# Kernel tuning notes

Measured on AMD Instinct MI355X. Metric: run time of the kernel, lower is better.

The kernel has to match this reference:

```python
import jax, jax.numpy as jnp
import numpy as np

B, T = 16, 100
MCL = 100      # MAX_CODE_LEN
D_IN = 200     # input_dim (= ques_encoding)
D_BERT = 768
KC = 50        # KC_one_hot_dim
KCD = 100      # kc_embed_dim
HID = 128
SCALE_BERT = 100
TW = 0.5       # QPALA_config.total_attention_weight
BTW = 0.5      # BLAA_config.total_attention_weight


def setup_inputs():
    key = jax.random.key(0)
    ks = jax.random.split(key, 20)
    f32 = jnp.float32
    # composite input feature vector: [ques_enc | code2vec idx | bert | time | score | kc one-hot]
    rnn_first = (jax.random.uniform(ks[0], (B, T, D_IN)) < 0.1).astype(f32)
    c2v = jax.random.randint(ks[1], (B, T, 3 * MCL), 0, 10000).astype(f32)
    bert = jax.random.normal(ks[2], (B, T, D_BERT), f32)
    time_f = jax.random.uniform(ks[3], (B, T, 10), f32)
    score_f = jax.random.uniform(ks[4], (B, T, 2), f32)
    kc = (jax.random.uniform(ks[5], (B, T, KC)) < 0.15).astype(f32)
    x = jnp.concatenate([rnn_first, c2v, bert, time_f, score_f, kc], axis=2)  # [B,T,1330]
    s = 0.05
    p = lambda k, shp: jax.random.normal(k, shp, f32) * s
    return dict(
        x=x,
        node_emb=p(ks[6], (10002, 100)),
        path_emb=p(ks[7], (20002, 100)),
        Wb=p(ks[8], (SCALE_BERT, D_BERT)), bb=jnp.zeros((SCALE_BERT,), f32),
        Wna=p(ks[9], (500, 500)), bna=jnp.zeros((500,), f32),
        Wia=p(ks[10], (KCD, 500)), bia=jnp.zeros((KCD,), f32),
        Wattn=p(ks[11], (1, 500)), battn=jnp.zeros((1,), f32),
        kc_emb=p(ks[12], (KC, KCD)),
        Wt=p(ks[13], (1, SCALE_BERT + KC + KCD)), bt=jnp.zeros((1,), f32),
        Wih=p(ks[14], (4 * HID, 950)), Whh=p(ks[15], (4 * HID, HID)),
        bih=jnp.zeros((4 * HID,), f32), bhh=jnp.zeros((4 * HID,), f32),
        Wfc=p(ks[16], (100, HID + KC + D_IN)), bfc=jnp.zeros((100,), f32),
    )


def _lstm(xseq, Wih, Whh, bih, bhh):
    # PyTorch LSTM, gate order i,f,g,o; batch_first
    bsz = xseq.shape[0]
    pre = jnp.einsum('btd,gd->btg', xseq, Wih) + bih + bhh  # [B,T,4H]

    def step(carry, g_in):
        h, c = carry
        g = g_in + h @ Whh.T
        i, f, gg, o = jnp.split(g, 4, axis=-1)
        c = jax.nn.sigmoid(f) * c + jax.nn.sigmoid(i) * jnp.tanh(gg)
        h = jax.nn.sigmoid(o) * jnp.tanh(c)
        return (h, c), h

    init = (jnp.zeros((bsz, HID), xseq.dtype), jnp.zeros((bsz, HID), xseq.dtype))
    _, hs = jax.lax.scan(step, init, jnp.swapaxes(pre, 0, 1))
    return jnp.swapaxes(hs, 0, 1)


def _forward(x, node_emb, path_emb, Wb, bb, Wna, bna, Wia, bia, Wattn, battn,
             kc_emb, Wt, bt, Wih, Whh, bih, bhh, Wfc, bfc):
    b, t = x.shape[0], x.shape[1]
    rnn_first = x[:, :, :D_IN]
    bert = x[:, :, 500:500 + D_BERT]
    kc_part = x[:, :, 1280:1280 + KC]
    c2v = x[:, :, D_IN:D_IN + 3 * MCL].reshape(b, t, MCL, 3).astype(jnp.int32)
    # gather embeddings + broadcast encoding -> full_embed [B,T,MCL,500]
    full = jnp.concatenate([
        node_emb[c2v[..., 0]], node_emb[c2v[..., 2]], path_emb[c2v[..., 1]],
        jnp.broadcast_to(rnn_first[:, :, None, :], (b, t, MCL, D_IN))], axis=3)
    bert_vec = bert @ Wb.T + bb  # [B,T,100]
    # non-interactive attention pooling (NB: original softmaxes over dim=1 = time)
    cw = jnp.tanh(full @ Wna.T + bna) @ Wattn.T + battn  # [B,T,MCL,1]
    aw = jax.nn.softmax(cw, axis=1)
    na = jnp.sum(full * aw, axis=2)  # [B,T,500]
    kcn = jnp.sum(kc_part, axis=2, keepdims=True)
    kcn = jnp.where(kcn == 0, 1.0, kcn)
    # interactive (KC) cross attention
    trans = full @ Wia.T + bia  # [B,T,MCL,KCD]
    Q = kc_part[..., None] * kc_emb[None, None]  # [B,T,KC,KCD]
    attn = jax.nn.softmax(jnp.einsum('btkd,btmd->btkm', Q, trans), axis=-1)
    Hm = jnp.einsum('btkm,btmd->btkd', attn, trans) * kc_part[..., None]
    ia = jnp.sum(Hm, axis=2) / kcn  # [B,T,KCD]
    rnn_input = jnp.concatenate([kc_part, rnn_first, ia, na, bert_vec], axis=2)  # [B,T,950]
    lstm_out = _lstm(rnn_input, Wih, Whh, bih, bhh)  # [B,T,HID]
    # per-time-step causal attention over lstm_out (vectorized form of the python loop)
    w = (jnp.concatenate([bert_vec, kc_part, ia], axis=2) @ Wt.T + bt)[..., 0]  # [B,T]
    mask = jnp.tril(jnp.ones((t, t), bool))
    logits = jnp.where(mask[None], w[:, None, :], -1e30)
    cattn = jax.nn.softmax(logits, axis=-1)  # [B,T,T]
    cur = jnp.einsum('bij,bjh->bih', cattn, lstm_out)
    attended = lstm_out * (1.0 - TW)
    attended = attended.at[:, 0].set(lstm_out[:, 0])
    idx = jnp.arange(t)
    addm = ((idx >= 1) & (idx <= t - 2)).astype(x.dtype)[None, :, None]
    attended = attended + cur * BTW * addm
    out = jax.nn.sigmoid(
        jnp.concatenate([rnn_first, kc_part, attended], axis=2) @ Wfc.T + bfc)
    return out  # [B,T,100]


def reference(x, node_emb, path_emb, Wb, bb, Wna, bna, Wia, bia, Wattn, battn,
              kc_emb, Wt, bt, Wih, Whh, bih, bhh, Wfc, bfc):
    return _forward(x, node_emb, path_emb, Wb, bb, Wna, bna, Wia, bia, Wattn, battn,
                    kc_emb, Wt, bt, Wih, Whh, bih, bhh, Wfc, bfc)
```

## Files before the change

### kernel.cpp

```cpp
#include <hip/hip_runtime.h>
#include <math.h>

typedef unsigned short ushort_t;
typedef __attribute__((ext_vector_type(8))) short bf16x8;
typedef __attribute__((ext_vector_type(4))) float f32x4;

constexpr int CB = 16, CT = 100, CMCL = 100, CDIN = 200;
constexpr int CKC = 50, CHID = 128;
constexpr int XCH = 1330;
constexpr int NBT = CB * CT;
constexpr int NNODE = 10002, NPATH = 20002;
constexpr int TRS = 114;
constexpr int HSTR = 136;
constexpr int NODE_W = 1408;
constexpr int PATH_W = 768;
constexpr int XR_W   = 640;

__device__ __forceinline__ float frcp(float v){ return __builtin_amdgcn_rcpf(v); }
__device__ __forceinline__ float fsigmoid(float v){ return frcp(1.f + __expf(-v)); }
__device__ __forceinline__ float ftanh_(float v){
  float e = __expf(-2.f*fabsf(v));
  return copysignf((1.f - e) * frcp(1.f + e), v);
}
__device__ __forceinline__ float wredsum(float v){
  #pragma unroll
  for (int off = 32; off; off >>= 1) v += __shfl_xor(v, off);
  return v;
}
__device__ __forceinline__ float wredmax(float v){
  #pragma unroll
  for (int off = 32; off; off >>= 1) v = fmaxf(v, __shfl_xor(v, off));
  return v;
}
__device__ __forceinline__ ushort_t f2b(float f){
  union { float f; unsigned u; } c{f};
  return (ushort_t)((c.u + 0x7FFFu + ((c.u >> 16) & 1u)) >> 16);
}
__device__ __forceinline__ float b2f(unsigned hbits){
  union { unsigned u; float f; } c{hbits << 16};
  return c.f;
}
__device__ __forceinline__ void b8f(const ushort_t* p, float* o){
  uint4 v = *reinterpret_cast<const uint4*>(p);
  o[0]=b2f(v.x & 0xFFFFu); o[1]=b2f(v.x >> 16);
  o[2]=b2f(v.y & 0xFFFFu); o[3]=b2f(v.y >> 16);
  o[4]=b2f(v.z & 0xFFFFu); o[5]=b2f(v.z >> 16);
  o[6]=b2f(v.w & 0xFFFFu); o[7]=b2f(v.w >> 16);
}

struct GDesc {
  const float* A; const float* B; float* Cf; ushort_t* Cb;
  int lda, kOff, kMax, K, M, Npad, rbp, cb, nsplit, ldc, blocks;
};
struct MegaArgs { GDesc d[4]; int nd; };

__global__ __launch_bounds__(256) void mega_gemm(MegaArgs args)
{
  constexpr int KS = 136;
  __shared__ ushort_t As[128*KS];
  __shared__ ushort_t Bs[128*KS];
  int id = blockIdx.x;
  int di = 0;
  while (di < args.nd-1 && id >= args.d[di].blocks) { id -= args.d[di].blocks; ++di; }
  GDesc g = args.d[di];
  const int per = g.rbp * g.cb;
  const int sp = id / per, r = id % per;
  const int xcd = r & 7, s2 = r >> 3;
  const int y = xcd + 8*(s2 / g.cb), cbi = s2 % g.cb;
  const int bm = y*128, bn = cbi*128;
  if (bm >= g.M) return;
  const int tid = threadIdx.x, lane = tid & 63, w = tid >> 6;
  const int wm = w & 1, wn = w >> 1;
  const int lr = lane & 15, lkq = lane >> 4;
  const int kbase = g.kOff + sp * g.K;
  const int hK = g.K >> 1;

  for (int f = tid; f < 128*hK; f += 256) {
    int row = f / hK, j2 = (f % hK)*2;
    int gm = bm + row;
    float2 va = make_float2(0.f,0.f);
    if (gm < g.M && kbase + j2 + 2 <= g.kMax)
      va = *reinterpret_cast<const float2*>(g.A + (long)gm*g.lda + kbase + j2);
    *reinterpret_cast<unsigned*>(&As[row*KS + j2]) = (unsigned)f2b(va.x) | ((unsigned)f2b(va.y)<<16);
    float2 vb = *reinterpret_cast<const float2*>(g.B + ((long)sp*g.Npad + bn + row)*g.K + j2);
    *reinterpret_cast<unsigned*>(&Bs[row*KS + j2]) = (unsigned)f2b(vb.x) | ((unsigned)f2b(vb.y)<<16);
  }
  const int padw = (128 - g.K) >> 1;
  for (int f = tid; f < 128*padw; f += 256) {
    int row = f / padw, jd = f % padw;
    *reinterpret_cast<unsigned*>(&As[row*KS + g.K + jd*2]) = 0u;
    *reinterpret_cast<unsigned*>(&Bs[row*KS + g.K + jd*2]) = 0u;
  }
  __syncthreads();

  f32x4 acc[4][4];
  #pragma unroll
  for (int i = 0; i < 4; ++i)
    #pragma unroll
    for (int j = 0; j < 4; ++j) acc[i][j] = f32x4{0.f,0.f,0.f,0.f};
  #pragma unroll
  for (int ks = 0; ks < 4; ++ks) {
    const int ko = ks*32 + lkq*8;
    bf16x8 af[4], bf[4];
    #pragma unroll
    for (int i = 0; i < 4; ++i)
      af[i] = *reinterpret_cast<const bf16x8*>(&As[(wm*64 + i*16 + lr)*KS + ko]);
    #pragma unroll
    for (int j = 0; j < 4; ++j)
      bf[j] = *reinterpret_cast<const bf16x8*>(&Bs[(wn*64 + j*16 + lr)*KS + ko]);
    #pragma unroll
    for (int i = 0; i < 4; ++i)
      #pragma unroll
      for (int j = 0; j < 4; ++j)
        acc[i][j] = __builtin_amdgcn_mfma_f32_16x16x32_bf16(af[i], bf[j], acc[i][j], 0, 0, 0);
  }
  #pragma unroll
  for (int i = 0; i < 4; ++i) {
    #pragma unroll
    for (int j = 0; j < 4; ++j) {
      #pragma unroll
      for (int rr = 0; rr < 4; ++rr) {
        int gr = bm + wm*64 + i*16 + lkq*4 + rr;
        int gc = bn + wn*64 + j*16 + lr;
        if (gr < g.M) {
          if (g.Cb) g.Cb[(long)gr * g.ldc + gc] = f2b(acc[i][j][rr]);
          else      g.Cf[((long)sp*g.M + gr)*g.ldc + gc] = acc[i][j][rr];
        }
      }
    }
  }
}

__global__ void pack_Bn(const float* __restrict__ Wna, const float* __restrict__ Wia, float* __restrict__ Bn)
{
  int i = blockIdx.x*256 + threadIdx.x;
  if (i >= NODE_W*100) return;
  int n = i / 100, k = i % 100;
  float v = 0.f;
  if (n < 500)                      v = Wna[(long)n*500 + k];
  else if (n >= 512 && n < 1012)    v = Wna[(long)(n-512)*500 + 100 + k];
  else if (n >= 1024 && n < 1124)   v = (k == n-1024) ? 1.f : 0.f;
  else if (n >= 1136 && n < 1236)   v = Wia[(long)(n-1136)*500 + k];
  else if (n >= 1248 && n < 1348)   v = Wia[(long)(n-1248)*500 + 100 + k];
  Bn[i] = v;
}
__global__ void pack_Bp(const float* __restrict__ Wna, const float* __restrict__ Wia, float* __restrict__ Bp)
{
  int i = blockIdx.x*256 + threadIdx.x;
  if (i >= PATH_W*100) return;
  int n = i / 100, k = i % 100;
  float v = 0.f;
  if (n < 500)                    v = Wna[(long)n*500 + 200 + k];
  else if (n >= 512 && n < 612)   v = (k == n-512) ? 1.f : 0.f;
  else if (n >= 624 && n < 724)   v = Wia[(long)(n-624)*500 + 200 + k];
  Bp[i] = v;
}
__global__ void pack_XB2(const float* __restrict__ Wna, const float* __restrict__ Wia,
                         const float* __restrict__ bna, const float* __restrict__ bia,
                         float* __restrict__ XB2, float* __restrict__ bias_x)
{
  int i = blockIdx.x*256 + threadIdx.x;
  if (i < XR_W) {
    float b = 0.f;
    if (i < 500) b = bna[i];
    else if (i >= 512 && i < 612) b = bia[i-512];
    bias_x[i] = b;
  }
  if (i >= 2*XR_W*100) return;
  int s = i / (XR_W*100), n = (i / 100) % XR_W, k = i % 100;
  int k2 = s*100 + k;
  float v = 0.f;
  if (n < 500)                  v = Wna[(long)n*500 + 300 + k2];
  else if (n >= 512 && n < 612) v = Wia[(long)(n-512)*500 + 300 + k2];
  XB2[i] = v;
}
__global__ void pack_bertB(const float* __restrict__ Wb, float* __restrict__ BertB)
{
  int i = blockIdx.x*256 + threadIdx.x;
  if (i >= 6*128*128) return;
  int s = i / (128*128), n = (i / 128) % 128, k = i % 128;
  BertB[i] = (n < 100) ? Wb[(long)n*768 + s*128 + k] : 0.f;
}
__global__ void pack_P2B(const float* __restrict__ Wih, float* __restrict__ P2B)
{
  int i = blockIdx.x*256 + threadIdx.x;
  if (i >= 10*512*96) return;
  int s = i / (512*96), n = (i / 96) % 512, k = i % 96;
  int kg = s*96 + k;
  P2B[i] = (kg < 950) ? Wih[(long)n*950 + kg] : 0.f;
}
__global__ void pack_wattn(const float* __restrict__ Wattn, ushort_t* __restrict__ wab)
{
  int i = blockIdx.x * 256 + threadIdx.x;
  if (i < 512) wab[i] = (i < 500) ? f2b(Wattn[i]) : (ushort_t)0;
}

__global__ __launch_bounds__(256) void reduce1(
    const float* __restrict__ xrP, const float* __restrict__ bias_x, ushort_t* __restrict__ XR,
    const float* __restrict__ bertP, const float* __restrict__ bb, float* __restrict__ rnn)
{
  int bt = blockIdx.x, tid = threadIdx.x;
  for (int c = tid; c < XR_W; c += 256) {
    float v = xrP[(long)bt*XR_W + c] + xrP[((long)NBT + bt)*XR_W + c] + bias_x[c];
    XR[(long)bt*XR_W + c] = f2b(v);
  }
  if (tid < 100) {
    float v = bb[tid];
    #pragma unroll
    for (int s = 0; s < 6; ++s) v += bertP[((long)s*NBT + bt)*128 + tid];
    rnn[(long)bt*950 + 850 + tid] = v;
  }
}

__global__ __launch_bounds__(512) void reduce_p2(
    const float* __restrict__ p2P, const float* __restrict__ bih, const float* __restrict__ bhh,
    ushort_t* __restrict__ P2)
{
  int bt = blockIdx.x, g = threadIdx.x;
  float v = bih[g] + bhh[g];
  #pragma unroll
  for (int s = 0; s < 10; ++s) v += p2P[((long)s*NBT + bt)*512 + g];
  int bq = bt / CT, tt = bt % CT;
  int q = g >> 7, rem = g & 127, ww = rem >> 4, lr2 = rem & 15;
  int lk2 = bq >> 2, rr = bq & 3;
  P2[((((long)tt*4 + q)*8 + ww)*4 + lk2)*64 + lr2*4 + rr] = f2b(v);
}

__global__ __launch_bounds__(256) void cw2_kernel(
    const float* __restrict__ x, const ushort_t* __restrict__ NODE_ALL,
    const ushort_t* __restrict__ PATH_ALL, const ushort_t* __restrict__ XR,
    const ushort_t* __restrict__ WAB,
    const float* __restrict__ battn, float* __restrict__ cwT)
{
  int bt = blockIdx.x, b = bt / CT, t = bt % CT;
  int tid = threadIdx.x, w = tid >> 6, lane = tid & 63;
  __shared__ int idx_s[300];
  for (int i = tid; i < 300; i += 256) idx_s[i] = (int)x[(long)bt*XCH + 200 + i];
  float rseg[8], wseg[8];
  b8f(XR + (long)bt*XR_W + lane*8, rseg);
  b8f(WAB + lane*8, wseg);
  __syncthreads();
  float bat = battn[0];

  uint4 A0, C0, P0, A1, C1, P1;
  auto issue = [&](int m, uint4& A, uint4& C, uint4& P){
    if (m < CMCL) {
      int ai = idx_s[3*m], pi = idx_s[3*m+1], ci = idx_s[3*m+2];
      A = *reinterpret_cast<const uint4*>(NODE_ALL + (long)ai*NODE_W + lane*8);
      C = *reinterpret_cast<const uint4*>(NODE_ALL + (long)ci*NODE_W + 512 + lane*8);
      P = *reinterpret_cast<const uint4*>(PATH_ALL + (long)pi*PATH_W + lane*8);
    }
  };
  auto proc = [&](int m, const uint4& A, const uint4& C, const uint4& P){
    if (m >= CMCL) return;
    const unsigned ua[4] = {A.x, A.y, A.z, A.w};
    const unsigned uc[4] = {C.x, C.y, C.z, C.w};
    const unsigned up[4] = {P.x, P.y, P.z, P.w};
    float acc = 0.f;
    #pragma unroll
    for (int jj = 0; jj < 4; ++jj) {
      float lo = b2f(ua[jj] & 0xffffu) + b2f(uc[jj] & 0xffffu) + b2f(up[jj] & 0xffffu) + rseg[2*jj];
      float hi = b2f(ua[jj] >> 16)     + b2f(uc[jj] >> 16)     + b2f(up[jj] >> 16)     + rseg[2*jj+1];
      acc = fmaf(ftanh_(lo), wseg[2*jj], acc);
      acc = fmaf(ftanh_(hi), wseg[2*jj+1], acc);
    }
    acc = wredsum(acc);
    if (lane == 0) cwT[((long)b*CMCL + m)*CT + t] = acc + bat;
  };

  issue(w, A0, C0, P0);
  for (int it = 0; it < 25; it += 2) {
    int m0 = w + it*4;
    issue(m0 + 4, A1, C1, P1);
    proc(m0, A0, C0, P0);
    issue(m0 + 8, A0, C0, P0);
    proc(m0 + 4, A1, C1, P1);
  }
}

__global__ void aw_kernel(const float* __restrict__ cwT, float* __restrict__ awT)
{
  int bm = blockIdx.x; int lane = threadIdx.x;
  const float* row = cwT + (long)bm * CT;
  bool h1 = lane < (CT - 64);
  float v0 = row[lane];
  float v1 = h1 ? row[64 + lane] : -3.0e38f;
  float mx = wredmax(fmaxf(v0, v1));
  float e0 = __expf(v0 - mx);
  float e1 = h1 ? __expf(v1 - mx) : 0.f;
  float s = wredsum(e0 + e1);
  float inv = frcp(s);
  awT[(long)bm*CT + lane] = e0 * inv;
  if (h1) awT[(long)bm*CT + 64 + lane] = e1 * inv;
}

__global__ __launch_bounds__(256) void fuse2_kernel(
    const float* __restrict__ x,
    const ushort_t* __restrict__ NODE_ALL, const ushort_t* __restrict__ PATH_ALL,
    const ushort_t* __restrict__ XR, const float* __restrict__ awT,
    const float* __restrict__ kc_emb, float* __restrict__ rnn)
{
  int bt = blockIdx.x, b = bt / CT, t = bt % CT;
  int tid = threadIdx.x, w = tid >> 6, lane = tid & 63;
  int sub = lane >> 5, li = lane & 31;

  __shared__ ushort_t tr_s[100*TRS];
  __shared__ float nacc[4][344];
  __shared__ float ia_red[4][104];
  __shared__ float aw_s[100];
  __shared__ int   idx_s[300];
  __shared__ float kcl[CKC];
  __shared__ int   act_k[CKC];
  __shared__ int   nact_s;
  __shared__ float kcn_s, awsum_s;

  for (int i = tid; i < 300; i += 256) idx_s[i] = (int)x[(long)bt*XCH + 200 + i];
  if (tid < 100) aw_s[tid] = awT[((long)b*CMCL + tid)*CT + t];
  if (tid < CKC) kcl[tid] = x[(long)bt*XCH + 1280 + tid];
  __syncthreads();
  if (tid == 0) {
    float kcn = 0.f; int na = 0;
    for (int k = 0; k < CKC; ++k) { float v = kcl[k]; kcn += v; if (v != 0.f) act_k[na++] = k; }
    nact_s = na; kcn_s = (kcn == 0.f) ? 1.f : kcn;
    float s = 0.f;
    for (int m = 0; m < CMCL; ++m) s += aw_s[m];
    awsum_s = s;
  }
  float rwseg[8];
  if (li >= 14 && li < 28) b8f(XR + (long)bt*XR_W + 512 + (li-14)*8, rwseg);
  __syncthreads();

  float na_a[8] = {}, na_c[8] = {}, na_p[8] = {};
  const bool gv = (li < 28);
  uint4 A0, C0, P0, A1, C1, P1;
  auto g_issue = [&](int m, uint4& A, uint4& C, uint4& P){
    if (m < CMCL && gv) {
      int ai = idx_s[3*m], pi = idx_s[3*m+1], ci = idx_s[3*m+2];
      int eo = li*8, uo = (li-14)*8;
      A = *reinterpret_cast<const uint4*>(NODE_ALL + (long)ai*NODE_W + 1024 + eo);
      C = *reinterpret_cast<const uint4*>(NODE_ALL + (long)ci*NODE_W + ((li<14) ? 1024 + eo : 1248 + uo));
      P = *reinterpret_cast<const uint4*>(PATH_ALL + (long)pi*PATH_W + 512 + eo);
    }
  };
  auto g_proc = [&](int m, const uint4& A, const uint4& C, const uint4& P){
    if (m >= CMCL || !gv) return;
    const unsigned ua[4] = {A.x, A.y, A.z, A.w};
    const unsigned uc[4] = {C.x, C.y, C.z, C.w};
    const unsigned up[4] = {P.x, P.y, P.z, P.w};
    if (li < 14) {
      float awm = aw_s[m];
      #pragma unroll
      for (int jj = 0; jj < 4; ++jj) {
        na_a[2*jj]   = fmaf(awm, b2f(ua[jj] & 0xffffu), na_a[2*jj]);
        na_a[2*jj+1] = fmaf(awm, b2f(ua[jj] >> 16),     na_a[2*jj+1]);
        na_c[2*jj]   = fmaf(awm, b2f(uc[jj] & 0xffffu), na_c[2*jj]);
        na_c[2*jj+1] = fmaf(awm, b2f(uc[jj] >> 16),     na_c[2*jj+1]);
        na_p[2*jj]   = fmaf(awm, b2f(up[jj] & 0xffffu), na_p[2*jj]);
        na_p[2*jj+1] = fmaf(awm, b2f(up[jj] >> 16),     na_p[2*jj+1]);
      }
    } else {
      unsigned* d32 = reinterpret_cast<unsigned*>(&tr_s[m*TRS + (li-14)*8]);
      #pragma unroll
      for (int jj = 0; jj < 4; ++jj) {
        float lo = b2f(ua[jj] & 0xffffu) + b2f(uc[jj] & 0xffffu) + b2f(up[jj] & 0xffffu) + rwseg[2*jj];
        float hi = b2f(ua[jj] >> 16)     + b2f(uc[jj] >> 16)     + b2f(up[jj] >> 16)     + rwseg[2*jj+1];
        d32[jj] = (unsigned)f2b(lo) | ((unsigned)f2b(hi) << 16);
      }
    }
  };
  const int mb = w*2 + sub;
  g_issue(mb, A0, C0, P0);
  for (int it = 0; it < 13; it += 2) {
    g_issue((it+1)*8 + mb, A1, C1, P1);
    g_proc(it*8 + mb, A0, C0, P0);
    g_issue((it+2)*8 + mb, A0, C0, P0);
    g_proc((it+1)*8 + mb, A1, C1, P1);
  }
  #pragma unroll
  for (int j = 0; j < 8; ++j) {
    na_a[j] += __shfl_xor(na_a[j], 32);
    na_c[j] += __shfl_xor(na_c[j], 32);
    na_p[j] += __shfl_xor(na_p[j], 32);
  }
  if (lane < 14) {
    #pragma unroll
    for (int j = 0; j < 8; ++j) {
      nacc[w][      lane*8 + j] = na_a[j];
      nacc[w][112 + lane*8 + j] = na_c[j];
      nacc[w][224 + lane*8 + j] = na_p[j];
    }
  }
  __syncthreads();

  for (int q = tid; q < 336; q += 256) {
    float v = nacc[0][q] + nacc[1][q] + nacc[2][q] + nacc[3][q];
    int seg = q / 112, col = q % 112;
    if (col < 100) rnn[(long)bt*950 + 350 + seg*100 + col] = v;
  }
  for (int q = tid; q < CDIN; q += 256) {
    float xv = x[(long)bt*XCH + q];
    rnn[(long)bt*950 + 50 + q] = xv;
    rnn[(long)bt*950 + 650 + q] = awsum_s * xv;
  }
  if (tid < CKC) rnn[(long)bt*950 + tid] = kcl[tid];

  float ia0 = 0.f, ia1 = 0.f;
  const bool vrow1 = lane < 36;
  const bool vpv   = lane < 50;
  const int nact = nact_s;
  const unsigned* tr32_0 = reinterpret_cast<const unsigned*>(&tr_s[lane*TRS]);
  const unsigned* tr32_1 = reinterpret_cast<const unsigned*>(&tr_s[(64+lane)*TRS]);
  const unsigned* tr32   = reinterpret_cast<const unsigned*>(tr_s);
  for (int ki = w; ki < nact; ki += 4) {
    int k = act_k[ki];
    float kck = kcl[k];
    const float* ke = kc_emb + (long)k*100;
    float s0 = 0.f, s1 = 0.f;
    #pragma unroll 5
    for (int dh = 0; dh < 50; ++dh) {
      float k0 = ke[2*dh], k1 = ke[2*dh+1];
      unsigned u0 = tr32_0[dh];
      s0 = fmaf(k0, b2f(u0 & 0xffffu), s0);
      s0 = fmaf(k1, b2f(u0 >> 16), s0);
      if (vrow1) {
        unsigned u1 = tr32_1[dh];
        s1 = fmaf(k0, b2f(u1 & 0xffffu), s1);
        s1 = fmaf(k1, b2f(u1 >> 16), s1);
      }
    }
    s0 *= kck; s1 *= kck;
    float mx = wredmax(fmaxf(s0, vrow1 ? s1 : -3.0e38f));
    float p0e = __expf(s0 - mx);
    float p1e = vrow1 ? __expf(s1 - mx) : 0.f;
    float sm = wredsum(p0e + p1e);
    float inv = kck * frcp(sm);
    p0e *= inv; p1e *= inv;
    #pragma unroll 4
    for (int m = 0; m < CMCL; ++m) {
      float pm = (m < 64) ? __shfl(p0e, m) : __shfl(p1e, m - 64);
      if (vpv) {
        unsigned u = tr32[m*57 + lane];
        ia0 = fmaf(pm, b2f(u & 0xffffu), ia0);
        ia1 = fmaf(pm, b2f(u >> 16), ia1);
      }
    }
  }
  if (vpv) { ia_red[w][2*lane] = ia0; ia_red[w][2*lane+1] = ia1; }
  __syncthreads();
  if (tid < 100) {
    float v = (ia_red[0][tid] + ia_red[1][tid] + ia_red[2][tid] + ia_red[3][tid]) * frcp(kcn_s);
    rnn[(long)bt*950 + 250 + tid] = v;
  }
}

__global__ __launch_bounds__(512) void lstm_mfma2(
    const ushort_t* __restrict__ P2,
    const float* __restrict__ Whh,
    float* __restrict__ lstm_out)
{
  const int tid = threadIdx.x, lane = tid & 63, w = tid >> 6;
  const int lr = lane & 15, lkq = lane >> 4;
  __shared__ ushort_t H[2][16 * HSTR];
  {
    ushort_t* hp = &H[0][0];
    for (int i = tid; i < 2*16*HSTR; i += 512) hp[i] = 0;
  }

  bf16x8 bw0[4], bw1[4], bw2[4], bw3[4];
  #pragma unroll
  for (int kk = 0; kk < 4; ++kk) {
    short s[8];
    const float* wp0 = Whh + (long)(0*128 + w*16 + lr) * 128 + kk*32 + lkq*8;
    const float* wp1 = Whh + (long)(1*128 + w*16 + lr) * 128 + kk*32 + lkq*8;
    const float* wp2 = Whh + (long)(2*128 + w*16 + lr) * 128 + kk*32 + lkq*8;
    const float* wp3 = Whh + (long)(3*128 + w*16 + lr) * 128 + kk*32 + lkq*8;
    #pragma unroll
    for (int j = 0; j < 8; ++j) s[j] = (short)f2b(wp0[j]);
    bw0[kk] = bf16x8{s[0],s[1],s[2],s[3],s[4],s[5],s[6],s[7]};
    #pragma unroll
    for (int j = 0; j < 8; ++j) s[j] = (short)f2b(wp1[j]);
    bw1[kk] = bf16x8{s[0],s[1],s[2],s[3],s[4],s[5],s[6],s[7]};
    #pragma unroll
    for (int j = 0; j < 8; ++j) s[j] = (short)f2b(wp2[j]);
    bw2[kk] = bf16x8{s[0],s[1],s[2],s[3],s[4],s[5],s[6],s[7]};
    #pragma unroll
    for (int j = 0; j < 8; ++j) s[j] = (short)f2b(wp3[j]);
    bw3[kk] = bf16x8{s[0],s[1],s[2],s[3],s[4],s[5],s[6],s[7]};
  }

  auto pptr = [&](int t, int q){
    return reinterpret_cast<const uint2*>(P2 + (((((long)t*4 + q)*8 + w)*4 + lkq)*64 + lr*4));
  };
  uint2 pc0 = *pptr(0,0), pc1 = *pptr(0,1), pc2 = *pptr(0,2), pc3 = *pptr(0,3);
  uint2 pn0, pn1, pn2, pn3;
  f32x4 c = {0.f,0.f,0.f,0.f};
  __syncthreads();

  int pb = 0;
  for (int t = 0; t < CT; ++t) {
    if (t + 1 < CT) { pn0 = *pptr(t+1,0); pn1 = *pptr(t+1,1); pn2 = *pptr(t+1,2); pn3 = *pptr(t+1,3); }
    bf16x8 a[4];
    #pragma unroll
    for (int kk = 0; kk < 4; ++kk)
      a[kk] = *reinterpret_cast<const bf16x8*>(&H[pb][lr*HSTR + kk*32 + lkq*8]);
    f32x4 acc0 = f32x4{ b2f(pc0.x & 0xffffu), b2f(pc0.x >> 16), b2f(pc0.y & 0xffffu), b2f(pc0.y >> 16) };
    f32x4 acc1 = f32x4{ b2f(pc1.x & 0xffffu), b2f(pc1.x >> 16), b2f(pc1.y & 0xffffu), b2f(pc1.y >> 16) };
    f32x4 acc2 = f32x4{ b2f(pc2.x & 0xffffu), b2f(pc2.x >> 16), b2f(pc2.y & 0xffffu), b2f(pc2.y >> 16) };
    f32x4 acc3 = f32x4{ b2f(pc3.x & 0xffffu), b2f(pc3.x >> 16), b2f(pc3.y & 0xffffu), b2f(pc3.y >> 16) };
    #pragma unroll
    for (int kk = 0; kk < 4; ++kk) {
      acc0 = __builtin_amdgcn_mfma_f32_16x16x32_bf16(a[kk], bw0[kk], acc0, 0,0,0);
      acc1 = __builtin_amdgcn_mfma_f32_16x16x32_bf16(a[kk], bw1[kk], acc1, 0,0,0);
      acc2 = __builtin_amdgcn_mfma_f32_16x16x32_bf16(a[kk], bw2[kk], acc2, 0,0,0);
      acc3 = __builtin_amdgcn_mfma_f32_16x16x32_bf16(a[kk], bw3[kk], acc3, 0,0,0);
    }
    #pragma unroll
    for (int r = 0; r < 4; ++r) {
      float ig = fsigmoid(acc0[r]);
      float fg = fsigmoid(acc1[r]);
      float gg = ftanh_(acc2[r]);
      float og = fsigmoid(acc3[r]);
      c[r] = fg*c[r] + ig*gg;
      float h = og * ftanh_(c[r]);
      int row = lkq*4 + r;
      H[pb^1][row*HSTR + w*16 + lr] = f2b(h);
      lstm_out[((long)row*CT + t)*128 + w*16 + lr] = h;
    }
    __syncthreads();
    pb ^= 1;
    pc0 = pn0; pc1 = pn1; pc2 = pn2; pc3 = pn3;
  }
}

__global__ void w_kernel(const float* __restrict__ rnn, const float* __restrict__ Wt,
                         const float* __restrict__ bt0, float* __restrict__ wbuf)
{
  int bt = blockIdx.x; int lane = threadIdx.x;
  float acc = 0.f;
  for (int i = lane; i < 250; i += 64) {
    float f;
    if (i < 100)      f = rnn[(long)bt*950 + 850 + i];
    else if (i < 150) f = rnn[(long)bt*950 + (i - 100)];
    else              f = rnn[(long)bt*950 + 250 + (i - 150)];
    acc = fmaf(Wt[i], f, acc);
  }
  acc = wredsum(acc);
  if (lane == 0) wbuf[bt] = acc + bt0[0];
}

__global__ void transpose_wfc(const float* __restrict__ Wfc, float* __restrict__ WfcT)
{
  int i = blockIdx.x*256 + threadIdx.x;
  if (i < 100*378) { int o = i / 378, q = i % 378; WfcT[q*100 + o] = Wfc[i]; }
}

__global__ __launch_bounds__(256) void final_kernel(
    const float* __restrict__ x, const float* __restrict__ wbuf,
    const float* __restrict__ lstm_out, const float* __restrict__ WfcT,
    const float* __restrict__ bfc, float* __restrict__ out)
{
  int bt = blockIdx.x; int b = bt / CT, i = bt % CT;
  int tid = threadIdx.x;
  __shared__ float p_s[CT];
  __shared__ float feat_s[384];
  if (tid < 64) {
    bool h1 = (64 + tid) < CT;
    float v0 = (tid <= i) ? wbuf[(long)b*CT + tid] : -3.0e38f;
    float v1 = (h1 && (64 + tid) <= i) ? wbuf[(long)b*CT + 64 + tid] : -3.0e38f;
    float mx = wredmax(fmaxf(v0, v1));
    float e0 = (tid <= i) ? __expf(v0 - mx) : 0.f;
    float e1 = (h1 && (64 + tid) <= i) ? __expf(v1 - mx) : 0.f;
    float s = wredsum(e0 + e1);
    float inv = frcp(s);
    p_s[tid] = e0 * inv;
    if (h1) p_s[64 + tid] = e1 * inv;
  }
  __syncthreads();
  if (tid < CHID) {
    float cur = 0.f;
    #pragma unroll 4
    for (int j = 0; j <= i; ++j) cur = fmaf(p_s[j], lstm_out[((long)b*CT + j)*CHID + tid], cur);
    float l = lstm_out[((long)b*CT + i)*CHID + tid];
    float att;
    if (i == 0) att = l;
    else { att = 0.5f * l; if (i <= CT - 2) att = fmaf(0.5f, cur, att); }
    feat_s[250 + tid] = att;
  }
  for (int q = tid; q < 250; q += 256)
    feat_s[q] = (q < 200) ? x[(long)bt*XCH + q] : x[(long)bt*XCH + 1280 + (q - 200)];
  __syncthreads();
  if (tid < 100) {
    float acc = bfc[tid];
    #pragma unroll 4
    for (int q = 0; q < 378; ++q) acc = fmaf(WfcT[q*100 + tid], feat_s[q], acc);
    out[(long)bt*100 + tid] = fsigmoid(acc);
  }
}

extern "C" void kernel_launch(void* const* d_in, const int* in_sizes, int n_in,
                              void* d_out, int out_size, void* d_ws, size_t ws_size,
                              hipStream_t stream) {
  (void)in_sizes; (void)n_in; (void)out_size; (void)ws_size;
  const float* x        = (const float*)d_in[0];
  const float* node_emb = (const float*)d_in[1];
  const float* path_emb = (const float*)d_in[2];
  const float* Wb       = (const float*)d_in[3];
  const float* bb       = (const float*)d_in[4];
  const float* Wna      = (const float*)d_in[5];
  const float* bna      = (const float*)d_in[6];
  const float* Wia      = (const float*)d_in[7];
  const float* bia      = (const float*)d_in[8];
  const float* Wattn    = (const float*)d_in[9];
  const float* battn    = (const float*)d_in[10];
  const float* kc_emb   = (const float*)d_in[11];
  const float* Wt       = (const float*)d_in[12];
  const float* bt0      = (const float*)d_in[13];
  const float* Wih      = (const float*)d_in[14];
  const float* Whh      = (const float*)d_in[15];
  const float* bih      = (const float*)d_in[16];
  const float* bhh      = (const float*)d_in[17];
  const float* Wfc      = (const float*)d_in[18];
  const float* bfc      = (const float*)d_in[19];
  float* out = (float*)d_out;

  char* cur = (char*)d_ws;
  auto alloc = [&](size_t bytes)->char* {
    char* p = cur; cur += (bytes + 255) & ~(size_t)255; return p;
  };
  ushort_t* NODE_ALL = (ushort_t*)alloc((size_t)NNODE*NODE_W*2);
  ushort_t* PATH_ALL = (ushort_t*)alloc((size_t)NPATH*PATH_W*2);
  ushort_t* XR   = (ushort_t*)alloc((size_t)NBT*XR_W*2);
  float* Bn     = (float*)alloc((size_t)NODE_W*100*4);
  float* Bp     = (float*)alloc((size_t)PATH_W*100*4);
  float* BertB  = (float*)alloc((size_t)6*128*128*4);
  float* XB2    = (float*)alloc((size_t)2*XR_W*100*4);
  float* P2B    = (float*)alloc((size_t)10*512*96*4);
  float* bias_x = (float*)alloc((size_t)XR_W*4);
  ushort_t* WAB = (ushort_t*)alloc(512*2);
  float* cwT  = (float*)alloc((size_t)NBT*100*4);
  float* awT  = (float*)alloc((size_t)NBT*100*4);
  float* rnn  = (float*)alloc((size_t)NBT*950*4);
  char*  uni  = alloc((size_t)10*NBT*512*4);
  float* xrP   = (float*)uni;
  float* bertP = (float*)(uni + (size_t)2*NBT*XR_W*4);
  float* p2P   = (float*)uni;
  ushort_t* P2 = (ushort_t*)alloc((size_t)NBT*512*2);
  float* lstm = (float*)alloc((size_t)NBT*128*4);
  float* wbuf = (float*)alloc((size_t)NBT*4);
  float* WfcT = (float*)alloc((size_t)378*100*4);

  pack_Bn<<<(NODE_W*100+255)/256, 256, 0, stream>>>(Wna, Wia, Bn);
  pack_Bp<<<(PATH_W*100+255)/256, 256, 0, stream>>>(Wna, Wia, Bp);
  pack_XB2<<<(2*XR_W*100+255)/256, 256, 0, stream>>>(Wna, Wia, bna, bia, XB2, bias_x);
  pack_bertB<<<(6*128*128+255)/256, 256, 0, stream>>>(Wb, BertB);
  pack_P2B<<<(10*512*96+255)/256, 256, 0, stream>>>(Wih, P2B);
  pack_wattn<<<2, 256, 0, stream>>>(Wattn, WAB);
  transpose_wfc<<<(100*378+255)/256,256,0,stream>>>(Wfc, WfcT);

  {
    MegaArgs a{};
    a.nd = 4;
    a.d[0] = { node_emb, Bn, nullptr, NODE_ALL, 100, 0, 100, 100, NNODE, NODE_W, 80, 11, 1, NODE_W, 80*11 };
    a.d[1] = { path_emb, Bp, nullptr, PATH_ALL, 100, 0, 100, 100, NPATH, PATH_W, 160, 6, 1, PATH_W, 160*6 };
    a.d[2] = { x, BertB, bertP, nullptr, XCH, 500, 1268, 128, NBT, 128, 16, 1, 6, 128, 16*1*6 };
    a.d[3] = { x, XB2, xrP, nullptr, XCH, 0, 200, 100, NBT, XR_W, 16, 5, 2, XR_W, 16*5*2 };
    int total = a.d[0].blocks + a.d[1].blocks + a.d[2].blocks + a.d[3].blocks;
    mega_gemm<<<total, 256, 0, stream>>>(a);
  }
  reduce1<<<NBT, 256, 0, stream>>>(xrP, bias_x, XR, bertP, bb, rnn);

  cw2_kernel<<<NBT,256,0,stream>>>(x, NODE_ALL, PATH_ALL, XR, WAB, battn, cwT);
  aw_kernel<<<CB*CMCL,64,0,stream>>>(cwT, awT);
  fuse2_kernel<<<NBT,256,0,stream>>>(x, NODE_ALL, PATH_ALL, XR, awT, kc_emb, rnn);

  {
    MegaArgs a{};
    a.nd = 1;
    a.d[0] = { rnn, P2B, p2P, nullptr, 950, 0, 950, 96, NBT, 512, 16, 4, 10, 512, 16*4*10 };
    mega_gemm<<<a.d[0].blocks, 256, 0, stream>>>(a);
  }
  reduce_p2<<<NBT, 512, 0, stream>>>(p2P, bih, bhh, P2);

  lstm_mfma2<<<1,512,0,stream>>>(P2, Whh, lstm);
  w_kernel<<<NBT,64,0,stream>>>(rnn, Wt, bt0, wbuf);
  final_kernel<<<NBT,256,0,stream>>>(x, wbuf, lstm, WfcT, bfc, out);
}
```

Before: 496.1 us.

## Merge weight packing kernels, fuse attention-weight dot into fuse2, widen node table

The seven separate weight-packing launches become one pack_all kernel, and the per-timestep Wt dot product moves from a standalone w_kernel into the tail of fuse2_kernel, reusing values already held in shared memory. The node embedding table is widened to give the child node's embedding its own identity block, so the gather loads become uniform with no lane-dependent address select. The goal is fewer kernel launches and less branching in the gather loop. In exchange the node GEMM gets more output columns, the table uses more memory, and fuse2 does more serial work at its end.

```diff
diff --git a/kernel.cpp b/kernel.cpp
--- a/kernel.cpp
+++ b/kernel.cpp
@@ -12,7 +12,7 @@
 constexpr int NNODE = 10002, NPATH = 20002;
 constexpr int TRS = 114;
 constexpr int HSTR = 136;
-constexpr int NODE_W = 1408;
+constexpr int NODE_W = 1536;
 constexpr int PATH_W = 768;
 constexpr int XR_W   = 640;
 
@@ -131,68 +131,74 @@
   }
 }
 
-__global__ void pack_Bn(const float* __restrict__ Wna, const float* __restrict__ Wia, float* __restrict__ Bn)
-{
-  int i = blockIdx.x*256 + threadIdx.x;
-  if (i >= NODE_W*100) return;
-  int n = i / 100, k = i % 100;
-  float v = 0.f;
-  if (n < 500)                      v = Wna[(long)n*500 + k];
-  else if (n >= 512 && n < 1012)    v = Wna[(long)(n-512)*500 + 100 + k];
-  else if (n >= 1024 && n < 1124)   v = (k == n-1024) ? 1.f : 0.f;
-  else if (n >= 1136 && n < 1236)   v = Wia[(long)(n-1136)*500 + k];
-  else if (n >= 1248 && n < 1348)   v = Wia[(long)(n-1248)*500 + 100 + k];
-  Bn[i] = v;
-}
-__global__ void pack_Bp(const float* __restrict__ Wna, const float* __restrict__ Wia, float* __restrict__ Bp)
-{
-  int i = blockIdx.x*256 + threadIdx.x;
-  if (i >= PATH_W*100) return;
-  int n = i / 100, k = i % 100;
-  float v = 0.f;
-  if (n < 500)                    v = Wna[(long)n*500 + 200 + k];
-  else if (n >= 512 && n < 612)   v = (k == n-512) ? 1.f : 0.f;
-  else if (n >= 624 && n < 724)   v = Wia[(long)(n-624)*500 + 200 + k];
-  Bp[i] = v;
-}
-__global__ void pack_XB2(const float* __restrict__ Wna, const float* __restrict__ Wia,
-                         const float* __restrict__ bna, const float* __restrict__ bia,
-                         float* __restrict__ XB2, float* __restrict__ bias_x)
-{
-  int i = blockIdx.x*256 + threadIdx.x;
-  if (i < XR_W) {
-    float b = 0.f;
-    if (i < 500) b = bna[i];
-    else if (i >= 512 && i < 612) b = bia[i-512];
-    bias_x[i] = b;
-  }
-  if (i >= 2*XR_W*100) return;
-  int s = i / (XR_W*100), n = (i / 100) % XR_W, k = i % 100;
-  int k2 = s*100 + k;
-  float v = 0.f;
-  if (n < 500)                  v = Wna[(long)n*500 + 300 + k2];
-  else if (n >= 512 && n < 612) v = Wia[(long)(n-512)*500 + 300 + k2];
-  XB2[i] = v;
-}
-__global__ void pack_bertB(const float* __restrict__ Wb, float* __restrict__ BertB)
-{
-  int i = blockIdx.x*256 + threadIdx.x;
-  if (i >= 6*128*128) return;
-  int s = i / (128*128), n = (i / 128) % 128, k = i % 128;
-  BertB[i] = (n < 100) ? Wb[(long)n*768 + s*128 + k] : 0.f;
-}
-__global__ void pack_P2B(const float* __restrict__ Wih, float* __restrict__ P2B)
-{
-  int i = blockIdx.x*256 + threadIdx.x;
-  if (i >= 10*512*96) return;
-  int s = i / (512*96), n = (i / 96) % 512, k = i % 96;
-  int kg = s*96 + k;
-  P2B[i] = (kg < 950) ? Wih[(long)n*950 + kg] : 0.f;
-}
-__global__ void pack_wattn(const float* __restrict__ Wattn, ushort_t* __restrict__ wab)
-{
-  int i = blockIdx.x * 256 + threadIdx.x;
-  if (i < 512) wab[i] = (i < 500) ? f2b(Wattn[i]) : (ushort_t)0;
+constexpr long PK_E0 = (long)NODE_W*100;
+constexpr long PK_E1 = PK_E0 + (long)PATH_W*100;
+constexpr long PK_E2 = PK_E1 + 2L*XR_W*100;
+constexpr long PK_E3 = PK_E2 + 6L*128*128;
+constexpr long PK_E4 = PK_E3 + 10L*512*96;
+constexpr long PK_E5 = PK_E4 + 512;
+constexpr long PK_E6 = PK_E5 + 378L*100;
+
+__global__ void pack_all(
+    const float* __restrict__ Wna, const float* __restrict__ Wia,
+    const float* __restrict__ bna, const float* __restrict__ bia,
+    const float* __restrict__ Wb, const float* __restrict__ Wih,
+    const float* __restrict__ Wattn, const float* __restrict__ Wfc,
+    float* __restrict__ Bn, float* __restrict__ Bp,
+    float* __restrict__ XB2, float* __restrict__ bias_x,
+    float* __restrict__ BertB, float* __restrict__ P2B,
+    ushort_t* __restrict__ WAB, float* __restrict__ WfcT)
+{
+  long i = (long)blockIdx.x*256 + threadIdx.x;
+  if (i < PK_E0) {
+    int n = (int)(i / 100), k = (int)(i % 100);
+    float v = 0.f;
+    if (n < 500)                      v = Wna[(long)n*500 + k];
+    else if (n >= 512 && n < 1012)    v = Wna[(long)(n-512)*500 + 100 + k];
+    else if (n >= 1024 && n < 1124)   v = (k == n-1024) ? 1.f : 0.f;
+    else if (n >= 1136 && n < 1236)   v = Wia[(long)(n-1136)*500 + k];
+    else if (n >= 1280 && n < 1380)   v = (k == n-1280) ? 1.f : 0.f;
+    else if (n >= 1392 && n < 1492)   v = Wia[(long)(n-1392)*500 + 100 + k];
+    Bn[i] = v;
+  } else if (i < PK_E1) {
+    long j = i - PK_E0;
+    int n = (int)(j / 100), k = (int)(j % 100);
+    float v = 0.f;
+    if (n < 500)                    v = Wna[(long)n*500 + 200 + k];
+    else if (n >= 512 && n < 612)   v = (k == n-512) ? 1.f : 0.f;
+    else if (n >= 624 && n < 724)   v = Wia[(long)(n-624)*500 + 200 + k];
+    Bp[j] = v;
+  } else if (i < PK_E2) {
+    long j = i - PK_E1;
+    if (j < XR_W) {
+      float b = 0.f;
+      if (j < 500) b = bna[j];
+      else if (j >= 512 && j < 612) b = bia[j-512];
+      bias_x[j] = b;
+    }
+    int s = (int)(j / (XR_W*100)), n = (int)((j / 100) % XR_W), k = (int)(j % 100);
+    int k2 = s*100 + k;
+    float v = 0.f;
+    if (n < 500)                  v = Wna[(long)n*500 + 300 + k2];
+    else if (n >= 512 && n < 612) v = Wia[(long)(n-512)*500 + 300 + k2];
+    XB2[j] = v;
+  } else if (i < PK_E3) {
+    long j = i - PK_E2;
+    int s = (int)(j / (128*128)), n = (int)((j / 128) % 128), k = (int)(j % 128);
+    BertB[j] = (n < 100) ? Wb[(long)n*768 + s*128 + k] : 0.f;
+  } else if (i < PK_E4) {
+    long j = i - PK_E3;
+    int s = (int)(j / (512*96)), n = (int)((j / 96) % 512), k = (int)(j % 96);
+    int kg = s*96 + k;
+    P2B[j] = (kg < 950) ? Wih[(long)n*950 + kg] : 0.f;
+  } else if (i < PK_E5) {
+    long j = i - PK_E4;
+    WAB[j] = (j < 500) ? f2b(Wattn[j]) : (ushort_t)0;
+  } else if (i < PK_E6) {
+    long j = i - PK_E5;
+    int o = (int)(j / 378), q = (int)(j % 378);
+    WfcT[q*100 + o] = Wfc[j];
+  }
 }
 
 __global__ __launch_bounds__(256) void reduce1(
@@ -298,7 +304,8 @@
     const float* __restrict__ x,
     const ushort_t* __restrict__ NODE_ALL, const ushort_t* __restrict__ PATH_ALL,
     const ushort_t* __restrict__ XR, const float* __restrict__ awT,
-    const float* __restrict__ kc_emb, float* __restrict__ rnn)
+    const float* __restrict__ kc_emb, float* __restrict__ rnn,
+    const float* __restrict__ Wt, const float* __restrict__ bt0, float* __restrict__ wbuf)
 {
   int bt = blockIdx.x, b = bt / CT, t = bt % CT;
   int tid = threadIdx.x, w = tid >> 6, lane = tid & 63;
@@ -307,6 +314,7 @@
   __shared__ ushort_t tr_s[100*TRS];
   __shared__ float nacc[4][344];
   __shared__ float ia_red[4][104];
+  __shared__ float ia_f[100];
   __shared__ float aw_s[100];
   __shared__ int   idx_s[300];
   __shared__ float kcl[CKC];
@@ -331,19 +339,17 @@
   __syncthreads();
 
   float na_a[8] = {}, na_c[8] = {}, na_p[8] = {};
-  const bool gv = (li < 28);
   uint4 A0, C0, P0, A1, C1, P1;
   auto g_issue = [&](int m, uint4& A, uint4& C, uint4& P){
-    if (m < CMCL && gv) {
+    if (m < CMCL) {
       int ai = idx_s[3*m], pi = idx_s[3*m+1], ci = idx_s[3*m+2];
-      int eo = li*8, uo = (li-14)*8;
-      A = *reinterpret_cast<const uint4*>(NODE_ALL + (long)ai*NODE_W + 1024 + eo);
-      C = *reinterpret_cast<const uint4*>(NODE_ALL + (long)ci*NODE_W + ((li<14) ? 1024 + eo : 1248 + uo));
-      P = *reinterpret_cast<const uint4*>(PATH_ALL + (long)pi*PATH_W + 512 + eo);
+      A = *reinterpret_cast<const uint4*>(NODE_ALL + (long)ai*NODE_W + 1024 + li*8);
+      C = *reinterpret_cast<const uint4*>(NODE_ALL + (long)ci*NODE_W + 1280 + li*8);
+      P = *reinterpret_cast<const uint4*>(PATH_ALL + (long)pi*PATH_W + 512  + li*8);
     }
   };
   auto g_proc = [&](int m, const uint4& A, const uint4& C, const uint4& P){
-    if (m >= CMCL || !gv) return;
+    if (m >= CMCL || li >= 28) return;
     const unsigned ua[4] = {A.x, A.y, A.z, A.w};
     const unsigned uc[4] = {C.x, C.y, C.z, C.w};
     const unsigned up[4] = {P.x, P.y, P.z, P.w};
@@ -450,6 +456,20 @@
   if (tid < 100) {
     float v = (ia_red[0][tid] + ia_red[1][tid] + ia_red[2][tid] + ia_red[3][tid]) * frcp(kcn_s);
     rnn[(long)bt*950 + 250 + tid] = v;
+    ia_f[tid] = v;
+  }
+  __syncthreads();
+  if (tid < 64) {
+    float acc = 0.f;
+    for (int i = tid; i < 250; i += 64) {
+      float f;
+      if (i < 100)      f = rnn[(long)bt*950 + 850 + i];
+      else if (i < 150) f = kcl[i - 100];
+      else              f = ia_f[i - 150];
+      acc = fmaf(Wt[i], f, acc);
+    }
+    acc = wredsum(acc);
+    if (tid == 0) wbuf[bt] = acc + bt0[0];
   }
 }
 
@@ -530,28 +550,6 @@
     pb ^= 1;
     pc0 = pn0; pc1 = pn1; pc2 = pn2; pc3 = pn3;
   }
-}
-
-__global__ void w_kernel(const float* __restrict__ rnn, const float* __restrict__ Wt,
-                         const float* __restrict__ bt0, float* __restrict__ wbuf)
-{
-  int bt = blockIdx.x; int lane = threadIdx.x;
-  float acc = 0.f;
-  for (int i = lane; i < 250; i += 64) {
-    float f;
-    if (i < 100)      f = rnn[(long)bt*950 + 850 + i];
-    else if (i < 150) f = rnn[(long)bt*950 + (i - 100)];
-    else              f = rnn[(long)bt*950 + 250 + (i - 150)];
-    acc = fmaf(Wt[i], f, acc);
-  }
-  acc = wredsum(acc);
-  if (lane == 0) wbuf[bt] = acc + bt0[0];
-}
-
-__global__ void transpose_wfc(const float* __restrict__ Wfc, float* __restrict__ WfcT)
-{
-  int i = blockIdx.x*256 + threadIdx.x;
-  if (i < 100*378) { int o = i / 378, q = i % 378; WfcT[q*100 + o] = Wfc[i]; }
 }
 
 __global__ __launch_bounds__(256) void final_kernel(
@@ -632,8 +630,8 @@
   ushort_t* XR   = (ushort_t*)alloc((size_t)NBT*XR_W*2);
   float* Bn     = (float*)alloc((size_t)NODE_W*100*4);
   float* Bp     = (float*)alloc((size_t)PATH_W*100*4);
+  float* XB2    = (float*)alloc((size_t)2*XR_W*100*4);
   float* BertB  = (float*)alloc((size_t)6*128*128*4);
-  float* XB2    = (float*)alloc((size_t)2*XR_W*100*4);
   float* P2B    = (float*)alloc((size_t)10*512*96*4);
   float* bias_x = (float*)alloc((size_t)XR_W*4);
   ushort_t* WAB = (ushort_t*)alloc(512*2);
@@ -649,18 +647,14 @@
   float* wbuf = (float*)alloc((size_t)NBT*4);
   float* WfcT = (float*)alloc((size_t)378*100*4);
 
-  pack_Bn<<<(NODE_W*100+255)/256, 256, 0, stream>>>(Wna, Wia, Bn);
-  pack_Bp<<<(PATH_W*100+255)/256, 256, 0, stream>>>(Wna, Wia, Bp);
-  pack_XB2<<<(2*XR_W*100+255)/256, 256, 0, stream>>>(Wna, Wia, bna, bia, XB2, bias_x);
-  pack_bertB<<<(6*128*128+255)/256, 256, 0, stream>>>(Wb, BertB);
-  pack_P2B<<<(10*512*96+255)/256, 256, 0, stream>>>(Wih, P2B);
-  pack_wattn<<<2, 256, 0, stream>>>(Wattn, WAB);
-  transpose_wfc<<<(100*378+255)/256,256,0,stream>>>(Wfc, WfcT);
+  pack_all<<<(unsigned)((PK_E6 + 255)/256), 256, 0, stream>>>(
+      Wna, Wia, bna, bia, Wb, Wih, Wattn, Wfc,
+      Bn, Bp, XB2, bias_x, BertB, P2B, WAB, WfcT);
 
   {
     MegaArgs a{};
     a.nd = 4;
-    a.d[0] = { node_emb, Bn, nullptr, NODE_ALL, 100, 0, 100, 100, NNODE, NODE_W, 80, 11, 1, NODE_W, 80*11 };
+    a.d[0] = { node_emb, Bn, nullptr, NODE_ALL, 100, 0, 100, 100, NNODE, NODE_W, 80, 12, 1, NODE_W, 80*12 };
     a.d[1] = { path_emb, Bp, nullptr, PATH_ALL, 100, 0, 100, 100, NPATH, PATH_W, 160, 6, 1, PATH_W, 160*6 };
     a.d[2] = { x, BertB, bertP, nullptr, XCH, 500, 1268, 128, NBT, 128, 16, 1, 6, 128, 16*1*6 };
     a.d[3] = { x, XB2, xrP, nullptr, XCH, 0, 200, 100, NBT, XR_W, 16, 5, 2, XR_W, 16*5*2 };
@@ -671,7 +665,7 @@
 
   cw2_kernel<<<NBT,256,0,stream>>>(x, NODE_ALL, PATH_ALL, XR, WAB, battn, cwT);
   aw_kernel<<<CB*CMCL,64,0,stream>>>(cwT, awT);
-  fuse2_kernel<<<NBT,256,0,stream>>>(x, NODE_ALL, PATH_ALL, XR, awT, kc_emb, rnn);
+  fuse2_kernel<<<NBT,256,0,stream>>>(x, NODE_ALL, PATH_ALL, XR, awT, kc_emb, rnn, Wt, bt0, wbuf);
 
   {
     MegaArgs a{};
@@ -682,6 +676,5 @@
   reduce_p2<<<NBT, 512, 0, stream>>>(p2P, bih, bhh, P2);
 
   lstm_mfma2<<<1,512,0,stream>>>(P2, Whh, lstm);
-  w_kernel<<<NBT,64,0,stream>>>(rnn, Wt, bt0, wbuf);
   final_kernel<<<NBT,256,0,stream>>>(x, wbuf, lstm, WfcT, bfc, out);
 }
```

Result: faster. 485.7 us (-2.1%).
